# Optimization experiments

Hardware: AMD Instinct MI355X
Metric: run time of the kernel (lower is better)

The kernel has to match this reference:

```python
import jax, jax.numpy as jnp
import numpy as np

SAMPLE_NUMS = 9
VIEW_RANGE = 2      # args.max_turn_view_range
TEMP = 0.07         # args.temperature
AVG_EPS = 1e-6      # BertAVG eps
COS_EPS = 1e-8      # torch.cosine_similarity eps


def setup_inputs() -> dict:
    key = jax.random.key(0)
    k0, k1, k2 = jax.random.split(key, 3)
    G, S, H = 8, 512, 768            # groups, max_seq_length, hidden_size
    B = G * SAMPLE_NUMS              # 72 flattened dialogues
    self_output = jax.random.normal(k0, (B, S, H), dtype=jnp.float32)
    attention_mask = jnp.ones((B, S), dtype=jnp.float32)
    qa_ids = jax.random.randint(k1, (B, S), 0, 4, dtype=jnp.int32)
    turn_ids = jnp.sort(jax.random.randint(k2, (B, S), 0, 16, dtype=jnp.int32), axis=-1)
    labels = jnp.zeros((G, SAMPLE_NUMS), dtype=jnp.float32).at[:, 0].set(1.0)
    return {"self_output": self_output, "attention_mask": attention_mask,
            "labels": labels, "qa_ids": qa_ids, "turn_ids": turn_ids}


def _masked_avg(x, m):
    # BertAVG: sum over seq of x*m / (sum(m) + eps)   x:[B,S,H] m:[B,S]
    return jnp.sum(x * m[..., None], axis=1) / (jnp.sum(m, axis=1, keepdims=True) + AVG_EPS)


def _cos(x, y):
    # torch.cosine_similarity over last dim, eps-clamped norms
    dot = jnp.sum(x * y, axis=-1)
    nx = jnp.maximum(jnp.linalg.norm(x, axis=-1), COS_EPS)
    ny = jnp.maximum(jnp.linalg.norm(y, axis=-1), COS_EPS)
    c = dot / (nx * ny)
    c = jnp.where(c == 1.0, jnp.nan, c)   # cos[cos==1] = nan
    return c / TEMP


def _calc_loss(pred, labels):
    return -jnp.nanmean(jax.nn.log_softmax(pred, axis=-1) * labels)


def reference(self_output, attention_mask, labels, qa_ids, turn_ids):
    H = self_output.shape[-1]
    # role masks from qa_ids
    q_mask = ((qa_ids == 1) | (qa_ids == 2)).astype(self_output.dtype)
    a_mask = ((qa_ids == 0) | (qa_ids == 2)).astype(self_output.dtype)
    n_mask = (qa_ids == 3).astype(self_output.dtype)
    q_am = attention_mask * q_mask
    a_am = attention_mask * a_mask
    n_am = attention_mask * n_mask
    q_so = self_output * q_am[..., None]   # [B,S,H]
    a_so = self_output * a_am[..., None]
    n_so = self_output * n_am[..., None]
    # role-masked cross scores [B,S,S]
    q_w = jnp.einsum('bsh,bth->bst', q_so, a_so + n_so)
    a_w = jnp.einsum('bsh,bth->bst', a_so, q_so + n_so)
    n_w = jnp.einsum('bsh,bth->bst', n_so, q_so + a_so)
    # turn-range band mask: |turn_s - turn_t| <= range
    dt = turn_ids[:, :, None] - turn_ids[:, None, :]
    band = (jnp.abs(dt) <= VIEW_RANGE).astype(self_output.dtype)  # [B,S,S]
    filtered_w = (q_w + a_w + n_w) * band
    # cross outputs
    q_co = jnp.einsum('bst,bth->bsh', filtered_w, q_so)
    a_co = jnp.einsum('bst,bth->bsh', filtered_w, a_so)
    n_co = jnp.einsum('bst,bth->bsh', filtered_w, n_so)
    # masked averages
    q_self = _masked_avg(q_so, q_am)
    q_cross = _masked_avg(q_co, a_am + n_am)
    a_self = _masked_avg(a_so, a_am)
    a_cross = _masked_avg(a_co, q_am + n_am)
    n_self = _masked_avg(n_so, n_am)
    n_cross = _masked_avg(n_co, q_am + a_am)
    # [G, sample_nums, H]
    q_self = q_self.reshape(-1, SAMPLE_NUMS, H)
    q_cross = q_cross.reshape(-1, SAMPLE_NUMS, H)
    a_self = a_self.reshape(-1, SAMPLE_NUMS, H)
    a_cross = a_cross.reshape(-1, SAMPLE_NUMS, H)
    n_self = n_self.reshape(-1, SAMPLE_NUMS, H)
    n_cross = n_cross.reshape(-1, SAMPLE_NUMS, H)
    q_output = q_self[:, 0, :]
    a_output = a_self[:, 0, :]
    n_output = n_self[:, 0, :]
    # vectorized over sample axis (replaces the python loop + stack)
    logit_q = _cos(q_self, q_cross)  # [G, sample_nums]
    logit_a = _cos(a_self, a_cross)
    logit_n = _cos(n_self, n_cross)
    stage_loss = (_calc_loss(logit_a, labels) + _calc_loss(logit_q, labels)
                  + _calc_loss(logit_n, labels)) / 3.0
    return (stage_loss, q_output, a_output, n_output)
```

## Files before the change

kernel.cpp:

```cpp
#include <hip/hip_runtime.h>
#include <math.h>

#define BB 72
#define SS 512
#define HH 768
#define GG 8
#define SN 9
#define VR 2
#define NT 16
#define NPART 16


__device__ float g_G[(size_t)BB * NT * 4 * HH];
__device__ float g_xpart[(size_t)BB * NPART * 3 * HH];
__device__ float g_logits[3 * BB];

__device__ __forceinline__ void class_masks(float am, int id, float& qv, float& av, float& nv) {
    qv = (id == 1 || id == 2) ? am : 0.0f;
    av = (id == 0 || id == 2) ? am : 0.0f;
    nv = (id == 3) ? am : 0.0f;
}

__global__ __launch_bounds__(192) void k_g(const float* __restrict__ x,
                                           const float* __restrict__ am,
                                           const int* __restrict__ qa,
                                           const int* __restrict__ turn) {
    __shared__ int   tn[SS];
    __shared__ float c2[SS];
    __shared__ int   idv[SS];

    const int u = blockIdx.x, b = blockIdx.y;
    const int tid = threadIdx.x;

    for (int i = tid; i < SS; i += 192) {
        tn[i] = turn[b * SS + i];
        float a = am[b * SS + i]; c2[i] = a * a;
        idv[i] = qa[b * SS + i];
    }
    __syncthreads();

    int L = 0, R = SS;
    while (L < R) { int m = (L + R) >> 1; if (tn[m] < u) L = m + 1; else R = m; }
    const int beg = L;
    L = 0; R = SS;
    while (L < R) { int m = (L + R) >> 1; if (tn[m] <= u) L = m + 1; else R = m; }
    const int end = L;

    float4 acc[4];
#pragma unroll
    for (int i = 0; i < 4; ++i) acc[i] = make_float4(0.f, 0.f, 0.f, 0.f);

    const float* xb = x + (size_t)b * SS * HH + tid * 4;
    for (int s = beg; s < end; s += 4) {
        float4 v[4];
#pragma unroll
        for (int k = 0; k < 4; ++k) {
            const int ss = s + k;
            v[k] = (ss < end) ? *(const float4*)(xb + (size_t)ss * HH)
                              : make_float4(0.f, 0.f, 0.f, 0.f);
        }
#pragma unroll
        for (int k = 0; k < 4; ++k) {
            const int ss = s + k;
            if (ss < end) {
                const float cc = c2[ss];
                const int id = idv[ss];
                const float4 xv = v[k];
                if (id == 0) { acc[0].x += xv.x * cc; acc[0].y += xv.y * cc;
                               acc[0].z += xv.z * cc; acc[0].w += xv.w * cc; }
                else if (id == 1) { acc[1].x += xv.x * cc; acc[1].y += xv.y * cc;
                                    acc[1].z += xv.z * cc; acc[1].w += xv.w * cc; }
                else if (id == 2) { acc[2].x += xv.x * cc; acc[2].y += xv.y * cc;
                                    acc[2].z += xv.z * cc; acc[2].w += xv.w * cc; }
                else { acc[3].x += xv.x * cc; acc[3].y += xv.y * cc;
                       acc[3].z += xv.z * cc; acc[3].w += xv.w * cc; }
            }
        }
    }

    float* go = g_G + ((size_t)(b * NT + u) * 4) * HH + tid * 4;
#pragma unroll
    for (int i = 0; i < 4; ++i)
        *(float4*)(go + (size_t)i * HH) = acc[i];
}

__global__ __launch_bounds__(256) void k_ct(const float* __restrict__ x,
                                            const float* __restrict__ am,
                                            const int* __restrict__ qa,
                                            const int* __restrict__ turn) {
    __shared__ float red[4][3 * HH];
    __shared__ int   tnb[32];
    __shared__ float amb[32];
    __shared__ int   idb[32];

    const int b = blockIdx.y, ts = blockIdx.x, T0 = ts * 32;
    const int tid = threadIdx.x, w = tid >> 6, lane = tid & 63;
    if (tid < 32) {
        tnb[tid] = turn[b * SS + T0 + tid];
        amb[tid] = am[b * SS + T0 + tid];
        idb[tid] = qa[b * SS + T0 + tid];
    }
    __syncthreads();

    const float* xb = x + (size_t)b * SS * HH;
    float4 xt[8][3];
#pragma unroll
    for (int it = 0; it < 8; ++it) {
        const float* xr = xb + (size_t)(T0 + w * 8 + it) * HH + lane * 4;
        xt[it][0] = *(const float4*)(xr + 0);
        xt[it][1] = *(const float4*)(xr + 256);
        xt[it][2] = *(const float4*)(xr + 512);
    }

    float xn[3][12];
#pragma unroll
    for (int c = 0; c < 3; ++c)
#pragma unroll
        for (int k = 0; k < 12; ++k) xn[c][k] = 0.0f;

    float4 Wr[4][3];
    int curv = -1;

#pragma unroll
    for (int it = 0; it < 8; ++it) {
        const int tl = w * 8 + it;
        const int v = tnb[tl];
        if (v != curv) {
            curv = v;
            const int ulo = (v - VR < 0) ? 0 : v - VR;
            const int uhi = (v + VR > NT - 1) ? NT - 1 : v + VR;
#pragma unroll
            for (int i = 0; i < 4; ++i)
#pragma unroll
                for (int ch = 0; ch < 3; ++ch)
                    Wr[i][ch] = make_float4(0.f, 0.f, 0.f, 0.f);
            for (int u = ulo; u <= uhi; ++u) {
                const float* Gg = g_G + ((size_t)(b * NT + u) * 4) * HH + lane * 4;
#pragma unroll
                for (int i = 0; i < 4; ++i) {
#pragma unroll
                    for (int ch = 0; ch < 3; ++ch) {
                        const float4 gv = *(const float4*)(Gg + (size_t)i * HH + ch * 256);
                        Wr[i][ch].x += gv.x; Wr[i][ch].y += gv.y;
                        Wr[i][ch].z += gv.z; Wr[i][ch].w += gv.w;
                    }
                }
            }
        }
        float d[4];
#pragma unroll
        for (int i = 0; i < 4; ++i) {
            float s = 0;
#pragma unroll
            for (int ch = 0; ch < 3; ++ch) {
                s += xt[it][ch].x * Wr[i][ch].x + xt[it][ch].y * Wr[i][ch].y
                   + xt[it][ch].z * Wr[i][ch].z + xt[it][ch].w * Wr[i][ch].w;
            }
            d[i] = s;
        }
#pragma unroll
        for (int off = 32; off; off >>= 1) {
#pragma unroll
            for (int i = 0; i < 4; ++i) d[i] += __shfl_xor(d[i], off);
        }
        float qt, at, nt; class_masks(amb[tl], idb[tl], qt, at, nt);
        const float ant = at + nt, qnt = qt + nt, qat = qt + at;
        const float Sqq = d[1] + d[2], Sqa = d[2], Saa = d[0] + d[2], Snn = d[3];
        const float cwq = qt * (ant * Sqa + qnt * Saa + qat * Snn);
        const float cwa = at * (ant * Sqq + qnt * Sqa + qat * Snn);
        const float cwn = nt * (ant * (Sqq + Sqa) + qnt * (Sqa + Saa));
#pragma unroll
        for (int ch = 0; ch < 3; ++ch) {
            const float4 xv = xt[it][ch];
            xn[0][ch * 4 + 0] += cwq * xv.x; xn[0][ch * 4 + 1] += cwq * xv.y;
            xn[0][ch * 4 + 2] += cwq * xv.z; xn[0][ch * 4 + 3] += cwq * xv.w;
            xn[1][ch * 4 + 0] += cwa * xv.x; xn[1][ch * 4 + 1] += cwa * xv.y;
            xn[1][ch * 4 + 2] += cwa * xv.z; xn[1][ch * 4 + 3] += cwa * xv.w;
            xn[2][ch * 4 + 0] += cwn * xv.x; xn[2][ch * 4 + 1] += cwn * xv.y;
            xn[2][ch * 4 + 2] += cwn * xv.z; xn[2][ch * 4 + 3] += cwn * xv.w;
        }
    }

#pragma unroll
    for (int c = 0; c < 3; ++c) {
#pragma unroll
        for (int ch = 0; ch < 3; ++ch) {
            float4 o;
            o.x = xn[c][ch * 4 + 0]; o.y = xn[c][ch * 4 + 1];
            o.z = xn[c][ch * 4 + 2]; o.w = xn[c][ch * 4 + 3];
            *(float4*)&red[w][c * HH + ch * 256 + lane * 4] = o;
        }
    }
    __syncthreads();
    float* xo = g_xpart + (size_t)(b * NPART + ts) * 3 * HH;
    for (int idx = tid * 4; idx < 3 * HH; idx += 1024) {
        float4 r0 = *(float4*)&red[0][idx];
        float4 r1 = *(float4*)&red[1][idx];
        float4 r2 = *(float4*)&red[2][idx];
        float4 r3 = *(float4*)&red[3][idx];
        float4 o;
        o.x = r0.x + r1.x + r2.x + r3.x;
        o.y = r0.y + r1.y + r2.y + r3.y;
        o.z = r0.z + r1.z + r2.z + r3.z;
        o.w = r0.w + r1.w + r2.w + r3.w;
        *(float4*)(xo + idx) = o;
    }
}

__global__ void k_cos(const float* __restrict__ am, const int* __restrict__ qa,
                      float* __restrict__ out) {
    const int c = blockIdx.x, b = blockIdx.y, tid = threadIdx.x;
    const int wave = tid >> 6, lane = tid & 63;
    __shared__ float redd[4][3];
    __shared__ float sD[3];

    float q = 0, a = 0, n = 0;
    for (int s = tid; s < SS; s += 256) {
        float m = am[b * SS + s]; int id = qa[b * SS + s];
        float qv, av, nv; class_masks(m, id, qv, av, nv);
        q += qv; a += av; n += nv;
    }
#pragma unroll
    for (int off = 32; off; off >>= 1) {
        q += __shfl_down(q, off); a += __shfl_down(a, off); n += __shfl_down(n, off);
    }
    if (lane == 0) { redd[wave][0] = q; redd[wave][1] = a; redd[wave][2] = n; }
    __syncthreads();
    if (tid == 0) {
        float Q = 0, A = 0, N = 0;
#pragma unroll
        for (int w = 0; w < 4; ++w) { Q += redd[w][0]; A += redd[w][1]; N += redd[w][2]; }
        sD[0] = Q; sD[1] = A; sD[2] = N;
    }
    __syncthreads();
    const float Dq = sD[0], Da = sD[1], Dn = sD[2];
    const float Dself = (c == 0) ? Dq : ((c == 1) ? Da : Dn);
    const float Dcross = (c == 0) ? (Da + Dn) : ((c == 1) ? (Dq + Dn) : (Dq + Da));
    const float invS = 1.0f / (Dself + 1e-6f), invC = 1.0f / (Dcross + 1e-6f);

    float dot = 0, n1 = 0, n2 = 0;
#pragma unroll
    for (int j = 0; j < 3; ++j) {
        const int h = tid + j * 256;
        const float* Gb = g_G + ((size_t)b * NT * 4) * HH + h;
        float sv = 0;
        if (c == 0) {
            for (int u = 0; u < NT; ++u)
                sv += Gb[(size_t)(u * 4 + 1) * HH] + Gb[(size_t)(u * 4 + 2) * HH];
        } else if (c == 1) {
            for (int u = 0; u < NT; ++u)
                sv += Gb[(size_t)(u * 4 + 0) * HH] + Gb[(size_t)(u * 4 + 2) * HH];
        } else {
            for (int u = 0; u < NT; ++u)
                sv += Gb[(size_t)(u * 4 + 3) * HH];
        }
        float cv = 0;
        const float* xp = g_xpart + ((size_t)b * NPART * 3 + c) * HH + h;
#pragma unroll
        for (int p = 0; p < NPART; ++p) cv += xp[(size_t)p * 3 * HH];
        sv *= invS; cv *= invC;
        dot += sv * cv; n1 += sv * sv; n2 += cv * cv;
        if (b % SN == 0)
            out[1 + ((size_t)c * GG + b / SN) * HH + h] = sv;
    }
#pragma unroll
    for (int off = 32; off; off >>= 1) {
        dot += __shfl_down(dot, off); n1 += __shfl_down(n1, off); n2 += __shfl_down(n2, off);
    }
    __shared__ float red2[4][3];
    if (lane == 0) { red2[wave][0] = dot; red2[wave][1] = n1; red2[wave][2] = n2; }
    __syncthreads();
    if (tid == 0) {
        float D = 0, N1 = 0, N2 = 0;
#pragma unroll
        for (int w = 0; w < 4; ++w) { D += red2[w][0]; N1 += red2[w][1]; N2 += red2[w][2]; }
        float nx = fmaxf(sqrtf(N1), 1e-8f);
        float ny = fmaxf(sqrtf(N2), 1e-8f);
        float cc = D / (nx * ny);
        if (cc == 1.0f) cc = __uint_as_float(0x7FC00000u);
        g_logits[c * BB + b] = cc / 0.07f;
    }
}

__global__ void k_loss(const float* __restrict__ labels, float* __restrict__ out) {
    __shared__ float rs[24];
    __shared__ int rc[24];
    const int tid = threadIdx.x;
    if (tid < 24) {
        int c = tid / GG, g = tid % GG;
        float lg[SN]; bool anynan = false;
        for (int j = 0; j < SN; ++j) {
            float v = g_logits[c * BB + g * SN + j];
            lg[j] = v;
            anynan = anynan || isnan(v);
        }
        float ssum = 0; int cnt = 0;
        if (!anynan) {
            float m = -1e30f;
            for (int j = 0; j < SN; ++j) m = fmaxf(m, lg[j]);
            float se = 0;
            for (int j = 0; j < SN; ++j) se += expf(lg[j] - m);
            float lse = m + logf(se);
            for (int j = 0; j < SN; ++j) ssum += (lg[j] - lse) * labels[g * SN + j];
            cnt = SN;
        }
        rs[tid] = ssum; rc[tid] = cnt;
    }
    __syncthreads();
    if (tid == 0) {
        float total = 0;
        for (int c = 0; c < 3; ++c) {
            float s = 0; int n = 0;
            for (int g = 0; g < GG; ++g) { s += rs[c * GG + g]; n += rc[c * GG + g]; }
            total += -(s / (float)n);
        }
        out[0] = total / 3.0f;
    }
}

extern "C" void kernel_launch(void* const* d_in, const int* in_sizes, int n_in,
                              void* d_out, int out_size, void* d_ws, size_t ws_size,
                              hipStream_t stream) {
    const float* x      = (const float*)d_in[0];
    const float* am     = (const float*)d_in[1];
    const float* labels = (const float*)d_in[2];
    const int*   qa     = (const int*)d_in[3];
    const int*   turn   = (const int*)d_in[4];
    float* out = (float*)d_out;

    k_g   <<<dim3(NT, BB),      192, 0, stream>>>(x, am, qa, turn);
    k_ct  <<<dim3(SS / 32, BB), 256, 0, stream>>>(x, am, qa, turn);
    k_cos <<<dim3(3, BB),       256, 0, stream>>>(am, qa, out);
    k_loss<<<dim3(1),           64,  0, stream>>>(labels, out);
}
```

Baseline: 280.2 us.

## Precompute windowed turn sums in new kernel and shrink k_ct reduction buffer

Adds a k_w kernel that precomputes the sliding-window sum of per-turn G vectors once per dialogue, so k_ct loads one W vector set per turn change instead of summing up to five G blocks. k_ct's per-wave shared reduction is replaced by shared-memory atomicAdd into a single buffer, cutting LDS use to raise occupancy. k_g now loads masks only for its turn range, narrows the second binary search, and unrolls its loads by 8. The cost is an extra launch, an extra global buffer round-trip, and atomic contention in LDS.

```diff
diff --git a/kernel.cpp b/kernel.cpp
--- a/kernel.cpp
+++ b/kernel.cpp
@@ -11,7 +11,8 @@
 #define NPART 16
 
 
-__device__ float g_G[(size_t)BB * NT * 4 * HH];
+__device__ float g_G [(size_t)BB * NT * 4 * HH];
+__device__ float g_Wm[(size_t)BB * NT * 4 * HH];
 __device__ float g_xpart[(size_t)BB * NPART * 3 * HH];
 __device__ float g_logits[3 * BB];
 
@@ -32,35 +33,37 @@
     const int u = blockIdx.x, b = blockIdx.y;
     const int tid = threadIdx.x;
 
-    for (int i = tid; i < SS; i += 192) {
-        tn[i] = turn[b * SS + i];
-        float a = am[b * SS + i]; c2[i] = a * a;
-        idv[i] = qa[b * SS + i];
-    }
+    for (int i = tid; i < SS; i += 192) tn[i] = turn[b * SS + i];
     __syncthreads();
 
     int L = 0, R = SS;
     while (L < R) { int m = (L + R) >> 1; if (tn[m] < u) L = m + 1; else R = m; }
     const int beg = L;
-    L = 0; R = SS;
+    L = beg; R = SS;
     while (L < R) { int m = (L + R) >> 1; if (tn[m] <= u) L = m + 1; else R = m; }
     const int end = L;
 
+    for (int i = beg + tid; i < end; i += 192) {
+        float a = am[b * SS + i]; c2[i] = a * a;
+        idv[i] = qa[b * SS + i];
+    }
+    __syncthreads();
+
     float4 acc[4];
 #pragma unroll
     for (int i = 0; i < 4; ++i) acc[i] = make_float4(0.f, 0.f, 0.f, 0.f);
 
     const float* xb = x + (size_t)b * SS * HH + tid * 4;
-    for (int s = beg; s < end; s += 4) {
-        float4 v[4];
-#pragma unroll
-        for (int k = 0; k < 4; ++k) {
+    for (int s = beg; s < end; s += 8) {
+        float4 v[8];
+#pragma unroll
+        for (int k = 0; k < 8; ++k) {
             const int ss = s + k;
             v[k] = (ss < end) ? *(const float4*)(xb + (size_t)ss * HH)
                               : make_float4(0.f, 0.f, 0.f, 0.f);
         }
 #pragma unroll
-        for (int k = 0; k < 4; ++k) {
+        for (int k = 0; k < 8; ++k) {
             const int ss = s + k;
             if (ss < end) {
                 const float cc = c2[ss];
@@ -84,11 +87,37 @@
         *(float4*)(go + (size_t)i * HH) = acc[i];
 }
 
+__global__ __launch_bounds__(256) void k_w() {
+    __shared__ float Gl[NT * 4 * 192];
+    const int qh = blockIdx.x, b = blockIdx.y, tid = threadIdx.x;
+
+    for (int idx = tid * 4; idx < NT * 4 * 192; idx += 1024) {
+        const int u = idx / 768, rem = idx % 768;
+        const int i = rem / 192, hh = rem % 192;
+        *(float4*)&Gl[idx] =
+            *(const float4*)(g_G + ((size_t)(b * NT + u) * 4 + i) * HH + qh * 192 + hh);
+    }
+    __syncthreads();
+
+    for (int idx = tid * 4; idx < NT * 4 * 192; idx += 1024) {
+        const int v = idx / 768, rem = idx % 768;
+        const int i = rem / 192, hh = rem % 192;
+        const int ulo = (v - VR < 0) ? 0 : v - VR;
+        const int uhi = (v + VR > NT - 1) ? NT - 1 : v + VR;
+        float4 s = make_float4(0.f, 0.f, 0.f, 0.f);
+        for (int u = ulo; u <= uhi; ++u) {
+            const float4 gv = *(const float4*)&Gl[(u * 4 + i) * 192 + hh];
+            s.x += gv.x; s.y += gv.y; s.z += gv.z; s.w += gv.w;
+        }
+        *(float4*)(g_Wm + ((size_t)(b * NT + v) * 4 + i) * HH + qh * 192 + hh) = s;
+    }
+}
+
 __global__ __launch_bounds__(256) void k_ct(const float* __restrict__ x,
                                             const float* __restrict__ am,
                                             const int* __restrict__ qa,
                                             const int* __restrict__ turn) {
-    __shared__ float red[4][3 * HH];
+    __shared__ float red[3 * HH];
     __shared__ int   tnb[32];
     __shared__ float amb[32];
     __shared__ int   idb[32];
@@ -100,6 +129,7 @@
         amb[tid] = am[b * SS + T0 + tid];
         idb[tid] = qa[b * SS + T0 + tid];
     }
+    for (int idx = tid; idx < 3 * HH; idx += 256) red[idx] = 0.0f;
     __syncthreads();
 
     const float* xb = x + (size_t)b * SS * HH;
@@ -127,24 +157,12 @@
         const int v = tnb[tl];
         if (v != curv) {
             curv = v;
-            const int ulo = (v - VR < 0) ? 0 : v - VR;
-            const int uhi = (v + VR > NT - 1) ? NT - 1 : v + VR;
-#pragma unroll
-            for (int i = 0; i < 4; ++i)
-#pragma unroll
-                for (int ch = 0; ch < 3; ++ch)
-                    Wr[i][ch] = make_float4(0.f, 0.f, 0.f, 0.f);
-            for (int u = ulo; u <= uhi; ++u) {
-                const float* Gg = g_G + ((size_t)(b * NT + u) * 4) * HH + lane * 4;
-#pragma unroll
-                for (int i = 0; i < 4; ++i) {
-#pragma unroll
-                    for (int ch = 0; ch < 3; ++ch) {
-                        const float4 gv = *(const float4*)(Gg + (size_t)i * HH + ch * 256);
-                        Wr[i][ch].x += gv.x; Wr[i][ch].y += gv.y;
-                        Wr[i][ch].z += gv.z; Wr[i][ch].w += gv.w;
-                    }
-                }
+            const float* Wg = g_Wm + ((size_t)(b * NT + v) * 4) * HH + lane * 4;
+#pragma unroll
+            for (int i = 0; i < 4; ++i) {
+                Wr[i][0] = *(const float4*)(Wg + (size_t)i * HH + 0);
+                Wr[i][1] = *(const float4*)(Wg + (size_t)i * HH + 256);
+                Wr[i][2] = *(const float4*)(Wg + (size_t)i * HH + 512);
             }
         }
         float d[4];
@@ -182,29 +200,17 @@
     }
 
 #pragma unroll
-    for (int c = 0; c < 3; ++c) {
-#pragma unroll
-        for (int ch = 0; ch < 3; ++ch) {
-            float4 o;
-            o.x = xn[c][ch * 4 + 0]; o.y = xn[c][ch * 4 + 1];
-            o.z = xn[c][ch * 4 + 2]; o.w = xn[c][ch * 4 + 3];
-            *(float4*)&red[w][c * HH + ch * 256 + lane * 4] = o;
-        }
-    }
-    __syncthreads();
+    for (int c = 0; c < 3; ++c)
+#pragma unroll
+        for (int ch = 0; ch < 3; ++ch)
+#pragma unroll
+            for (int k = 0; k < 4; ++k)
+                atomicAdd(&red[c * HH + ch * 256 + lane * 4 + k], xn[c][ch * 4 + k]);
+    __syncthreads();
+
     float* xo = g_xpart + (size_t)(b * NPART + ts) * 3 * HH;
-    for (int idx = tid * 4; idx < 3 * HH; idx += 1024) {
-        float4 r0 = *(float4*)&red[0][idx];
-        float4 r1 = *(float4*)&red[1][idx];
-        float4 r2 = *(float4*)&red[2][idx];
-        float4 r3 = *(float4*)&red[3][idx];
-        float4 o;
-        o.x = r0.x + r1.x + r2.x + r3.x;
-        o.y = r0.y + r1.y + r2.y + r3.y;
-        o.z = r0.z + r1.z + r2.z + r3.z;
-        o.w = r0.w + r1.w + r2.w + r3.w;
-        *(float4*)(xo + idx) = o;
-    }
+    for (int idx = tid * 4; idx < 3 * HH; idx += 1024)
+        *(float4*)(xo + idx) = *(float4*)&red[idx];
 }
 
 __global__ void k_cos(const float* __restrict__ am, const int* __restrict__ qa,
@@ -329,6 +335,7 @@
     float* out = (float*)d_out;
 
     k_g   <<<dim3(NT, BB),      192, 0, stream>>>(x, am, qa, turn);
+    k_w   <<<dim3(4, BB),       256, 0, stream>>>();
     k_ct  <<<dim3(SS / 32, BB), 256, 0, stream>>>(x, am, qa, turn);
     k_cos <<<dim3(3, BB),       256, 0, stream>>>(am, qa, out);
     k_loss<<<dim3(1),           64,  0, stream>>>(labels, out);
```

After: 292.0 us. 4.2% more time.
